# Kernel optimization log

Measured on AMD Instinct MI355X. Metric: run time of the kernel, lower is better.

Reference implementation:

```python
import jax, jax.numpy as jnp
import numpy as np

D_MODEL, D_STATE, D_CONV, EXPAND = 1024, 16, 4, 2
D_INNER = EXPAND * D_MODEL
B, L = 2, 2048
DT = 0.1  # module hard-codes dt = 0.1 (dt_proj is unused)


def setup_inputs() -> dict:
    key = jax.random.key(0)
    ks = jax.random.split(key, 7)
    s = 0.02
    x = jax.random.normal(ks[0], (B, L, D_MODEL), dtype=jnp.float32)
    in_proj_w = jax.random.normal(ks[1], (2 * D_INNER, D_MODEL), dtype=jnp.float32) * s
    conv_w = jax.random.normal(ks[2], (D_INNER, 1, D_CONV), dtype=jnp.float32) * s
    conv_b = jnp.zeros((D_INNER,), dtype=jnp.float32)
    x_proj_w = jax.random.normal(ks[3], (2 * D_STATE, D_INNER), dtype=jnp.float32) * s
    A_log = jnp.log(jnp.tile(jnp.arange(1, D_STATE + 1, dtype=jnp.float32), (D_INNER, 1)))
    D_param = jnp.ones((D_INNER,), dtype=jnp.float32)
    out_proj_w = jax.random.normal(ks[4], (D_MODEL, D_INNER), dtype=jnp.float32) * s
    return {"x": x, "in_proj_w": in_proj_w, "conv_w": conv_w, "conv_b": conv_b,
            "x_proj_w": x_proj_w, "A_log": A_log, "D_param": D_param,
            "out_proj_w": out_proj_w}


def _silu(v):
    return v * jax.nn.sigmoid(v)


def reference(x, in_proj_w, conv_w, conv_b, x_proj_w, A_log, D_param, out_proj_w):
    # in_proj: (B,L,d_model) -> (B,L,2*d_inner)
    xz = jnp.einsum('bld,ed->ble', x, in_proj_w)
    xs, z = jnp.split(xz, 2, axis=-1)
    # depthwise causal conv1d (torch pads both sides d_conv-1 then slices [:L] == left-pad only)
    xc = jax.lax.conv_general_dilated(
        xs.transpose(0, 2, 1), conv_w, window_strides=(1,),
        padding=[(D_CONV - 1, 0)], dimension_numbers=('NCH', 'OIH', 'NCH'),
        feature_group_count=D_INNER) + conv_b[None, :, None]
    xs = _silu(xc.transpose(0, 2, 1))  # (B, L, d_inner)
    # x_proj -> B_proj, C_proj  (B,L,d_state) each
    x_dbl = jnp.einsum('bld,ed->ble', xs, x_proj_w)
    B_proj, C_proj = jnp.split(x_dbl, 2, axis=-1)
    # SSM scan; dt is constant 0.1 so dA = exp(dt*A) is time-invariant
    A = -jnp.exp(A_log)                 # (d_inner, d_state)
    dA = jnp.exp(DT * A)                # (d_inner, d_state)

    def step(h, inp):
        x_t, B_t, C_t = inp             # (B,D), (B,N), (B,N)
        h = dA[None] * h + DT * B_t[:, None, :] * x_t[:, :, None]
        y_t = jnp.einsum('bdn,bn->bd', h, C_t)
        return h, y_t

    h0 = jnp.zeros((B, D_INNER, D_STATE), dtype=xs.dtype)
    _, ys = jax.lax.scan(step, h0,
                         (xs.transpose(1, 0, 2), B_proj.transpose(1, 0, 2), C_proj.transpose(1, 0, 2)))
    y = ys.transpose(1, 0, 2) + xs * D_param[None, None, :]
    y = y * _silu(z)
    return jnp.einsum('bld,ed->ble', y, out_proj_w)
```

## Files before the change

### kernel.cpp

```cpp
#include <hip/hip_runtime.h>
#include <hip/hip_bf16.h>
#include <math.h>

#define D_MODEL 1024
#define D_STATE 16
#define D_CONV  4
#define D_INNER 2048
#define BATCH   2
#define SEQ     2048
#define M_TOTAL (BATCH*SEQ)
#define DT_VAL  0.1f

#define CHUNK 64
#define WARM  64
#define NCHUNK (SEQ / CHUNK)
#define TSTEP 8

typedef __attribute__((ext_vector_type(8))) __bf16 bf16x8;
typedef __attribute__((ext_vector_type(4))) __bf16 bf16x4;
typedef __attribute__((ext_vector_type(4))) float floatx4;

__device__ __forceinline__ void gld_lds16(const __bf16* g, __bf16* l) {
    __builtin_amdgcn_global_load_lds(
        (const __attribute__((address_space(1))) void*)g,
        (__attribute__((address_space(3))) void*)l, 16, 0, 0);
}

template<int EPI>
__global__ __launch_bounds__(256) void gemm_v4(
    const __bf16* __restrict__ A, int lda,
    const __bf16* __restrict__ W, int ldw,
    float* __restrict__ Cf, int ldc,
    __bf16* __restrict__ O1, __bf16* __restrict__ O2,
    int nbx, int klen)
{
    __shared__ __bf16 As[2][128][32];
    __shared__ __bf16 Bs[2][128][32];

    const int tid  = threadIdx.x;
    const int bid  = blockIdx.x;
    const int xcd  = bid & 7;
    const int i    = bid >> 3;
    const int byl  = i & 3;
    const int rest = i >> 2;
    const int bx   = rest % nbx;
    const int ks   = rest / nbx;
    const int m0   = (xcd * 4 + byl) * 128;
    const int n0   = bx * 128;
    const int koff = ks * klen;

    const int wave = tid >> 6;
    const int lane = tid & 63;
    const int wr   = (wave >> 1) << 6;
    const int wc   = (wave & 1) << 6;
    const int fm   = lane & 15;
    const int fk   = (lane >> 4) << 3;
    const int grow = lane >> 2;
    const int gcol = (lane & 3) << 3;

    floatx4 acc[4][4];
    #pragma unroll
    for (int a = 0; a < 4; ++a)
        #pragma unroll
        for (int b = 0; b < 4; ++b)
            acc[a][b] = (floatx4){0.f, 0.f, 0.f, 0.f};

    for (int k0 = 0; k0 < klen; k0 += 64) {
        const int kg = koff + k0;
        __syncthreads();
        #pragma unroll
        for (int p = 0; p < 2; ++p) {
            #pragma unroll
            for (int issue = 0; issue < 2; ++issue) {
                const int r = issue * 64 + wave * 16 + grow;
                gld_lds16(A + (size_t)(m0 + r) * lda + kg + p * 32 + gcol,
                          &As[p][r][gcol]);
                gld_lds16(W + (size_t)(n0 + r) * ldw + kg + p * 32 + gcol,
                          &Bs[p][r][gcol]);
            }
        }
        __syncthreads();

        #pragma unroll
        for (int p = 0; p < 2; ++p) {
            bf16x8 af[4], bfv[4];
            #pragma unroll
            for (int a = 0; a < 4; ++a)
                af[a] = *(bf16x8*)&As[p][wr + a * 16 + fm][fk];
            #pragma unroll
            for (int b = 0; b < 4; ++b)
                bfv[b] = *(bf16x8*)&Bs[p][wc + b * 16 + fm][fk];
            #pragma unroll
            for (int a = 0; a < 4; ++a)
                #pragma unroll
                for (int b = 0; b < 4; ++b)
                    acc[a][b] = __builtin_amdgcn_mfma_f32_16x16x32_bf16(
                        af[a], bfv[b], acc[a][b], 0, 0, 0);
        }
    }

    const int crow = (lane >> 4) << 2;
    const int ccol = lane & 15;
    #pragma unroll
    for (int a = 0; a < 4; ++a) {
        #pragma unroll
        for (int b = 0; b < 4; ++b) {
            const int cm = m0 + wr + a * 16 + crow;
            const int cn = n0 + wc + b * 16 + ccol;
            #pragma unroll
            for (int r = 0; r < 4; ++r) {
                const float v = acc[a][b][r];
                if (EPI == 1) {
                    if (n0 < 2048) {
                        O1[(size_t)(cm + r) * 2048 + cn] = (__bf16)v;
                    } else {
                        const float s = v / (1.f + __expf(-v));
                        O2[(size_t)(cm + r) * 2048 + cn - 2048] = (__bf16)s;
                    }
                } else {
                    Cf[(size_t)ks * M_TOTAL * ldc + (size_t)(cm + r) * ldc + cn] = v;
                }
            }
        }
    }
}

__global__ __launch_bounds__(256) void reduce2(
    const float* __restrict__ p, float* __restrict__ out)
{
    const size_t i = (size_t)(blockIdx.x * 256 + threadIdx.x) * 4;
    const float4 a = *(const float4*)(p + i);
    const float4 b = *(const float4*)(p + (size_t)M_TOTAL * D_MODEL + i);
    float4 o;
    o.x = a.x + b.x; o.y = a.y + b.y; o.z = a.z + b.z; o.w = a.w + b.w;
    *(float4*)(out + i) = o;
}

__global__ __launch_bounds__(256) void xproj_mfma(
    const __bf16* __restrict__ X, const __bf16* __restrict__ Wp,
    float* __restrict__ bc)
{
    __shared__ __bf16 Ash[128][32];
    __shared__ __bf16 Wsh[32][264];

    const int tid  = threadIdx.x;
    const int bid  = blockIdx.x;
    const int ks   = bid & 7;
    const int mb   = bid >> 3;
    const int m0   = mb * 128;
    const int koff = ks * 256;
    const int wave = tid >> 6;
    const int lane = tid & 63;
    const int fm   = lane & 15;
    const int fk   = (lane >> 4) << 3;
    const int grow = lane >> 2;
    const int gcol = (lane & 3) << 3;

    {
        const int r = tid >> 3;
        const int c = (tid & 7) << 5;
        #pragma unroll
        for (int q = 0; q < 4; ++q)
            *(bf16x8*)&Wsh[r][c + q * 8] =
                *(const bf16x8*)(Wp + (size_t)r * D_INNER + koff + c + q * 8);
    }

    floatx4 acc[2][2];
    #pragma unroll
    for (int a = 0; a < 2; ++a)
        #pragma unroll
        for (int b = 0; b < 2; ++b)
            acc[a][b] = (floatx4){0.f, 0.f, 0.f, 0.f};

    for (int kit = 0; kit < 8; ++kit) {
        const int kg = koff + kit * 32;
        __syncthreads();
        #pragma unroll
        for (int issue = 0; issue < 2; ++issue) {
            const int r = issue * 64 + wave * 16 + grow;
            gld_lds16(X + (size_t)(m0 + r) * D_INNER + kg + gcol, &Ash[r][gcol]);
        }
        __syncthreads();

        bf16x8 af[2], wf[2];
        af[0] = *(bf16x8*)&Ash[wave * 32 + fm][fk];
        af[1] = *(bf16x8*)&Ash[wave * 32 + 16 + fm][fk];
        wf[0] = *(bf16x8*)&Wsh[fm][kit * 32 + fk];
        wf[1] = *(bf16x8*)&Wsh[16 + fm][kit * 32 + fk];
        #pragma unroll
        for (int a = 0; a < 2; ++a)
            #pragma unroll
            for (int b = 0; b < 2; ++b)
                acc[a][b] = __builtin_amdgcn_mfma_f32_16x16x32_bf16(
                    af[a], wf[b], acc[a][b], 0, 0, 0);
    }

    const int crow = (lane >> 4) << 2;
    const int ccol = lane & 15;
    #pragma unroll
    for (int a = 0; a < 2; ++a)
        #pragma unroll
        for (int b = 0; b < 2; ++b)
            #pragma unroll
            for (int r = 0; r < 4; ++r)
                atomicAdd(bc + (size_t)(m0 + wave * 32 + a * 16 + crow + r) * 32
                             + b * 16 + ccol, acc[a][b][r]);
}

__global__ __launch_bounds__(256) void cast4(
    const float* __restrict__ x, const float* __restrict__ win,
    const float* __restrict__ wout, const float* __restrict__ xpw,
    __bf16* __restrict__ xbf, __bf16* __restrict__ winbf,
    __bf16* __restrict__ woutbf, __bf16* __restrict__ xpwbf)
{
    const size_t j = (size_t)(blockIdx.x * 256 + threadIdx.x) * 4;
    const float* src; __bf16* dst; size_t off;
    if (j < 4194304)       { src = x;    dst = xbf;    off = j; }
    else if (j < 8388608)  { src = win;  dst = winbf;  off = j - 4194304; }
    else if (j < 10485760) { src = wout; dst = woutbf; off = j - 8388608; }
    else                   { src = xpw;  dst = xpwbf;  off = j - 10485760; }
    const float4 v = *(const float4*)(src + off);
    bf16x4 o;
    o[0] = (__bf16)v.x; o[1] = (__bf16)v.y; o[2] = (__bf16)v.z; o[3] = (__bf16)v.w;
    *(bf16x4*)(dst + off) = o;
}

__global__ __launch_bounds__(256) void conv_silu(
    const __bf16* __restrict__ xsp, const float* __restrict__ cw,
    const float* __restrict__ cb, __bf16* __restrict__ xsc)
{
    const int g  = blockIdx.x * 256 + threadIdx.x;
    const int d4 = g & (D_INNER / 4 - 1);
    const int m  = g >> 9;
    const int l  = m & (SEQ - 1);
    const int d  = d4 << 2;

    const float4 w0 = *(const float4*)(cw + (size_t)(d + 0) * 4);
    const float4 w1 = *(const float4*)(cw + (size_t)(d + 1) * 4);
    const float4 w2 = *(const float4*)(cw + (size_t)(d + 2) * 4);
    const float4 w3 = *(const float4*)(cw + (size_t)(d + 3) * 4);
    const float4 bv = *(const float4*)(cb + d);
    float a0 = bv.x, a1 = bv.y, a2 = bv.z, a3 = bv.w;

    #pragma unroll
    for (int j = 0; j < 4; ++j) {
        if (l + j >= 3) {
            const bf16x4 v = *(const bf16x4*)(xsp + (size_t)(m + j - 3) * D_INNER + d);
            const float wj0 = (j==0)?w0.x:(j==1)?w0.y:(j==2)?w0.z:w0.w;
            const float wj1 = (j==0)?w1.x:(j==1)?w1.y:(j==2)?w1.z:w1.w;
            const float wj2 = (j==0)?w2.x:(j==1)?w2.y:(j==2)?w2.z:w2.w;
            const float wj3 = (j==0)?w3.x:(j==1)?w3.y:(j==2)?w3.z:w3.w;
            a0 = fmaf(wj0, (float)v[0], a0);
            a1 = fmaf(wj1, (float)v[1], a1);
            a2 = fmaf(wj2, (float)v[2], a2);
            a3 = fmaf(wj3, (float)v[3], a3);
        }
    }
    a0 = a0 / (1.f + __expf(-a0));
    a1 = a1 / (1.f + __expf(-a1));
    a2 = a2 / (1.f + __expf(-a2));
    a3 = a3 / (1.f + __expf(-a3));
    bf16x4 ob;
    ob[0] = (__bf16)a0; ob[1] = (__bf16)a1; ob[2] = (__bf16)a2; ob[3] = (__bf16)a3;
    *(bf16x4*)(xsc + (size_t)m * D_INNER + d) = ob;
}

__global__ __launch_bounds__(256) void ssm_scan(
    const __bf16* __restrict__ xsc, const float* __restrict__ bc,
    const __bf16* __restrict__ szbf, __bf16* __restrict__ ybf,
    const float* __restrict__ alog, const float* __restrict__ dpar)
{
    __shared__ float Bsh[CHUNK + WARM][16];
    __shared__ float Csh[CHUNK + WARM][16];
    __shared__ float Xsh[2][TSTEP][256];
    __shared__ float Zsh[2][TSTEP][256];

    const int tid = threadIdx.x;
    const int blk = blockIdx.x;
    const int db  = blk & 7;
    const int ch  = (blk >> 3) & (NCHUNK - 1);
    const int b   = blk >> 8;
    const int d0  = db * 256;
    const int d   = d0 + tid;
    const int t0  = ch * CHUNK;
    const int tw  = (t0 >= WARM) ? (t0 - WARM) : 0;
    const int warm = t0 - tw;
    const int nt  = t0 + CHUNK - tw;
    const int ntiles = nt / TSTEP;

    const float* bcp = bc + ((size_t)b * SEQ + tw) * 32;
    for (int i = tid; i < nt * 8; i += 256) {
        const int row = i >> 3, q = i & 7;
        const float4 v = *(const float4*)(bcp + (size_t)row * 32 + q * 4);
        if (q < 4) *(float4*)&Bsh[row][q * 4] = v;
        else       *(float4*)&Csh[row][(q - 4) * 4] = v;
    }

    float dAv[16], h[16];
    #pragma unroll
    for (int q = 0; q < 4; ++q) {
        const float4 av = *(const float4*)(alog + (size_t)d * D_STATE + q * 4);
        dAv[q*4+0] = expf(-DT_VAL * expf(av.x));
        dAv[q*4+1] = expf(-DT_VAL * expf(av.y));
        dAv[q*4+2] = expf(-DT_VAL * expf(av.z));
        dAv[q*4+3] = expf(-DT_VAL * expf(av.w));
    }
    #pragma unroll
    for (int n = 0; n < 16; ++n) h[n] = 0.f;
    const float Dd = dpar[d];

    const __bf16* xbase = xsc  + ((size_t)b * SEQ + tw) * D_INNER + d0;
    const __bf16* zbase = szbf + ((size_t)b * SEQ + tw) * D_INNER + d0;
    __bf16*       ybase = ybf  + ((size_t)b * SEQ + tw) * D_INNER + d0;

    const int lrow = tid >> 6;
    const int lcol = (tid & 63) << 2;

    {
        const bf16x4 xa = *(const bf16x4*)(xbase + (size_t)lrow * D_INNER + lcol);
        const bf16x4 xb = *(const bf16x4*)(xbase + (size_t)(lrow + 4) * D_INNER + lcol);
        float4 fa, fb;
        fa.x=(float)xa[0]; fa.y=(float)xa[1]; fa.z=(float)xa[2]; fa.w=(float)xa[3];
        fb.x=(float)xb[0]; fb.y=(float)xb[1]; fb.z=(float)xb[2]; fb.w=(float)xb[3];
        *(float4*)&Xsh[0][lrow][lcol]     = fa;
        *(float4*)&Xsh[0][lrow + 4][lcol] = fb;
        if (warm == 0) {
            const bf16x4 za = *(const bf16x4*)(zbase + (size_t)lrow * D_INNER + lcol);
            const bf16x4 zb = *(const bf16x4*)(zbase + (size_t)(lrow + 4) * D_INNER + lcol);
            float4 ga, gb;
            ga.x=(float)za[0]; ga.y=(float)za[1]; ga.z=(float)za[2]; ga.w=(float)za[3];
            gb.x=(float)zb[0]; gb.y=(float)zb[1]; gb.z=(float)zb[2]; gb.w=(float)zb[3];
            *(float4*)&Zsh[0][lrow][lcol]     = ga;
            *(float4*)&Zsh[0][lrow + 4][lcol] = gb;
        }
    }
    __syncthreads();

    for (int tile = 0; tile < ntiles; ++tile) {
        const int buf = tile & 1;
        const int s   = tile * TSTEP;
        const int s2  = s + TSTEP;
        const bool more = (tile + 1 < ntiles);
        const bool znext = more && (s2 >= warm);

        bf16x4 rx0, rx1, rz0, rz1;
        if (more) {
            rx0 = *(const bf16x4*)(xbase + (size_t)(s2 + lrow) * D_INNER + lcol);
            rx1 = *(const bf16x4*)(xbase + (size_t)(s2 + lrow + 4) * D_INNER + lcol);
        }
        if (znext) {
            rz0 = *(const bf16x4*)(zbase + (size_t)(s2 + lrow) * D_INNER + lcol);
            rz1 = *(const bf16x4*)(zbase + (size_t)(s2 + lrow + 4) * D_INNER + lcol);
        }

        #pragma unroll
        for (int tt = 0; tt < TSTEP; ++tt) {
            const int t = s + tt;
            const float x   = Xsh[buf][tt][tid];
            const float dtx = DT_VAL * x;
            float y0 = 0.f, y1 = 0.f, y2 = 0.f, y3 = 0.f;
            #pragma unroll
            for (int n = 0; n < 4; ++n) {
                h[n]      = fmaf(dAv[n],      h[n],      dtx * Bsh[t][n]);
                h[n + 4]  = fmaf(dAv[n + 4],  h[n + 4],  dtx * Bsh[t][n + 4]);
                h[n + 8]  = fmaf(dAv[n + 8],  h[n + 8],  dtx * Bsh[t][n + 8]);
                h[n + 12] = fmaf(dAv[n + 12], h[n + 12], dtx * Bsh[t][n + 12]);
                y0 = fmaf(h[n],      Csh[t][n],      y0);
                y1 = fmaf(h[n + 4],  Csh[t][n + 4],  y1);
                y2 = fmaf(h[n + 8],  Csh[t][n + 8],  y2);
                y3 = fmaf(h[n + 12], Csh[t][n + 12], y3);
            }
            if (t >= warm) {
                const float sz = Zsh[buf][tt][tid];
                const float y  = fmaf(x, Dd, (y0 + y1) + (y2 + y3));
                ybase[(size_t)t * D_INNER + tid] = (__bf16)(y * sz);
            }
        }

        if (more) {
            float4 fa, fb;
            fa.x=(float)rx0[0]; fa.y=(float)rx0[1]; fa.z=(float)rx0[2]; fa.w=(float)rx0[3];
            fb.x=(float)rx1[0]; fb.y=(float)rx1[1]; fb.z=(float)rx1[2]; fb.w=(float)rx1[3];
            *(float4*)&Xsh[buf ^ 1][lrow][lcol]     = fa;
            *(float4*)&Xsh[buf ^ 1][lrow + 4][lcol] = fb;
        }
        if (znext) {
            float4 ga, gb;
            ga.x=(float)rz0[0]; ga.y=(float)rz0[1]; ga.z=(float)rz0[2]; ga.w=(float)rz0[3];
            gb.x=(float)rz1[0]; gb.y=(float)rz1[1]; gb.z=(float)rz1[2]; gb.w=(float)rz1[3];
            *(float4*)&Zsh[buf ^ 1][lrow][lcol]     = ga;
            *(float4*)&Zsh[buf ^ 1][lrow + 4][lcol] = gb;
        }
        __syncthreads();
    }
}

extern "C" void kernel_launch(void* const* d_in, const int* in_sizes, int n_in,
                              void* d_out, int out_size, void* d_ws, size_t ws_size,
                              hipStream_t stream)
{
    const float* x    = (const float*)d_in[0];
    const float* win  = (const float*)d_in[1];
    const float* cw   = (const float*)d_in[2];
    const float* cb   = (const float*)d_in[3];
    const float* xpw  = (const float*)d_in[4];
    const float* alog = (const float*)d_in[5];
    const float* dpar = (const float*)d_in[6];
    const float* wout = (const float*)d_in[7];
    float* out = (float*)d_out;

    char* w = (char*)d_ws;
    float*  pbuf   = (float*)w;
    __bf16* szbf   = (__bf16*)(w + 33554432);
    __bf16* xspbf  = (__bf16*)(w + 50331648);
    __bf16* xsc    = (__bf16*)(w + 67108864);
    float*  bcbuf  = (float*)(w + 83886080);
    __bf16* r1     = (__bf16*)(w + 84410368);
    __bf16* xbf    = r1;
    __bf16* winbf  = r1 + 4194304;
    __bf16* ybf    = r1;
    __bf16* woutbf = (__bf16*)(w + 101187584);
    __bf16* xpwbf  = (__bf16*)(w + 105381888);

    cast4<<<10304, 256, 0, stream>>>(x, win, wout, xpw, xbf, winbf, woutbf, xpwbf);
    hipMemsetAsync(bcbuf, 0, (size_t)M_TOTAL * 32 * 4, stream);
    gemm_v4<1><<<1024, 256, 0, stream>>>(
        xbf, D_MODEL, winbf, D_MODEL, nullptr, 0, xspbf, szbf, 32, 1024);
    conv_silu<<<(M_TOTAL * (D_INNER / 4)) / 256, 256, 0, stream>>>(
        xspbf, cw, cb, xsc);
    xproj_mfma<<<256, 256, 0, stream>>>(xsc, xpwbf, bcbuf);
    ssm_scan<<<BATCH * NCHUNK * 8, 256, 0, stream>>>(
        xsc, bcbuf, szbf, ybf, alog, dpar);
    gemm_v4<2><<<512, 256, 0, stream>>>(
        ybf, D_INNER, woutbf, D_INNER, pbuf, D_MODEL, nullptr, nullptr, 8, 1024);
    reduce2<<<(M_TOTAL * D_MODEL / 4) / 256, 256, 0, stream>>>(pbuf, out);
}
```

Baseline: 258.9 us.

## Use 256x128 tile GEMM for in_proj and fold bc memset into cast kernel

Adds a dedicated in_proj GEMM kernel with 256x128 output tiles per block (each wave computes 128x64), halving the block count to 512 and raising arithmetic intensity per LDS load. The zeroing of the B/C accumulation buffer moves from a separate hipMemsetAsync into extra threads of the cast kernel, removing one launch. The larger per-wave accumulator (32 MFMA tiles) raises register pressure and may reduce occupancy.

```diff
diff --git a/kernel.cpp b/kernel.cpp
--- a/kernel.cpp
+++ b/kernel.cpp
@@ -26,12 +26,101 @@
         (__attribute__((address_space(3))) void*)l, 16, 0, 0);
 }
 
-template<int EPI>
+__global__ __launch_bounds__(256) void gemm_inproj_fat(
+    const __bf16* __restrict__ A, const __bf16* __restrict__ W,
+    __bf16* __restrict__ O1, __bf16* __restrict__ O2)
+{
+    __shared__ __bf16 As[2][256][32];
+    __shared__ __bf16 Bs[2][128][32];
+
+    const int tid  = threadIdx.x;
+    const int bid  = blockIdx.x;
+    const int xcd  = bid & 7;
+    const int i    = bid >> 3;
+    const int byl  = i & 1;
+    const int bx   = i >> 1;
+    const int m0   = (xcd * 2 + byl) * 256;
+    const int n0   = bx * 128;
+
+    const int wave = tid >> 6;
+    const int lane = tid & 63;
+    const int wm   = (wave >> 1) << 7;
+    const int wn   = (wave & 1) << 6;
+    const int fm   = lane & 15;
+    const int fk   = (lane >> 4) << 3;
+    const int grow = lane >> 2;
+    const int gcol = (lane & 3) << 3;
+
+    floatx4 acc[8][4];
+    #pragma unroll
+    for (int a = 0; a < 8; ++a)
+        #pragma unroll
+        for (int b = 0; b < 4; ++b)
+            acc[a][b] = (floatx4){0.f, 0.f, 0.f, 0.f};
+
+    for (int kg = 0; kg < D_MODEL; kg += 64) {
+        __syncthreads();
+        #pragma unroll
+        for (int p = 0; p < 2; ++p) {
+            #pragma unroll
+            for (int issue = 0; issue < 4; ++issue) {
+                const int r = issue * 64 + wave * 16 + grow;
+                gld_lds16(A + (size_t)(m0 + r) * D_MODEL + kg + p * 32 + gcol,
+                          &As[p][r][gcol]);
+            }
+            #pragma unroll
+            for (int issue = 0; issue < 2; ++issue) {
+                const int r = issue * 64 + wave * 16 + grow;
+                gld_lds16(W + (size_t)(n0 + r) * D_MODEL + kg + p * 32 + gcol,
+                          &Bs[p][r][gcol]);
+            }
+        }
+        __syncthreads();
+
+        #pragma unroll
+        for (int p = 0; p < 2; ++p) {
+            bf16x8 af[8], bfv[4];
+            #pragma unroll
+            for (int a = 0; a < 8; ++a)
+                af[a] = *(bf16x8*)&As[p][wm + a * 16 + fm][fk];
+            #pragma unroll
+            for (int b = 0; b < 4; ++b)
+                bfv[b] = *(bf16x8*)&Bs[p][wn + b * 16 + fm][fk];
+            #pragma unroll
+            for (int a = 0; a < 8; ++a)
+                #pragma unroll
+                for (int b = 0; b < 4; ++b)
+                    acc[a][b] = __builtin_amdgcn_mfma_f32_16x16x32_bf16(
+                        af[a], bfv[b], acc[a][b], 0, 0, 0);
+        }
+    }
+
+    const int crow = (lane >> 4) << 2;
+    const int ccol = lane & 15;
+    #pragma unroll
+    for (int a = 0; a < 8; ++a) {
+        #pragma unroll
+        for (int b = 0; b < 4; ++b) {
+            const int cm = m0 + wm + a * 16 + crow;
+            const int cn = n0 + wn + b * 16 + ccol;
+            #pragma unroll
+            for (int r = 0; r < 4; ++r) {
+                const float v = acc[a][b][r];
+                if (n0 < 2048) {
+                    O1[(size_t)(cm + r) * 2048 + cn] = (__bf16)v;
+                } else {
+                    const float s = v / (1.f + __expf(-v));
+                    O2[(size_t)(cm + r) * 2048 + cn - 2048] = (__bf16)s;
+                }
+            }
+        }
+    }
+}
+
 __global__ __launch_bounds__(256) void gemm_v4(
     const __bf16* __restrict__ A, int lda,
     const __bf16* __restrict__ W, int ldw,
     float* __restrict__ Cf, int ldc,
-    __bf16* __restrict__ O1, __bf16* __restrict__ O2,
     int nbx, int klen)
 {
     __shared__ __bf16 As[2][128][32];
@@ -108,19 +197,9 @@
             const int cm = m0 + wr + a * 16 + crow;
             const int cn = n0 + wc + b * 16 + ccol;
             #pragma unroll
-            for (int r = 0; r < 4; ++r) {
-                const float v = acc[a][b][r];
-                if (EPI == 1) {
-                    if (n0 < 2048) {
-                        O1[(size_t)(cm + r) * 2048 + cn] = (__bf16)v;
-                    } else {
-                        const float s = v / (1.f + __expf(-v));
-                        O2[(size_t)(cm + r) * 2048 + cn - 2048] = (__bf16)s;
-                    }
-                } else {
-                    Cf[(size_t)ks * M_TOTAL * ldc + (size_t)(cm + r) * ldc + cn] = v;
-                }
-            }
+            for (int r = 0; r < 4; ++r)
+                Cf[(size_t)ks * M_TOTAL * ldc + (size_t)(cm + r) * ldc + cn] =
+                    acc[a][b][r];
         }
     }
 }
@@ -207,13 +286,20 @@
                              + b * 16 + ccol, acc[a][b][r]);
 }
 
-__global__ __launch_bounds__(256) void cast4(
+__global__ __launch_bounds__(256) void cast5(
     const float* __restrict__ x, const float* __restrict__ win,
     const float* __restrict__ wout, const float* __restrict__ xpw,
     __bf16* __restrict__ xbf, __bf16* __restrict__ winbf,
-    __bf16* __restrict__ woutbf, __bf16* __restrict__ xpwbf)
-{
-    const size_t j = (size_t)(blockIdx.x * 256 + threadIdx.x) * 4;
+    __bf16* __restrict__ woutbf, __bf16* __restrict__ xpwbf,
+    float* __restrict__ bcz)
+{
+    const size_t g = (size_t)(blockIdx.x * 256 + threadIdx.x);
+    if (g >= 2637824) {
+        const size_t off = (g - 2637824) * 4;
+        *(float4*)(bcz + off) = (float4){0.f, 0.f, 0.f, 0.f};
+        return;
+    }
+    const size_t j = g * 4;
     const float* src; __bf16* dst; size_t off;
     if (j < 4194304)       { src = x;    dst = xbf;    off = j; }
     else if (j < 8388608)  { src = win;  dst = winbf;  off = j - 4194304; }
@@ -422,16 +508,15 @@
     __bf16* woutbf = (__bf16*)(w + 101187584);
     __bf16* xpwbf  = (__bf16*)(w + 105381888);
 
-    cast4<<<10304, 256, 0, stream>>>(x, win, wout, xpw, xbf, winbf, woutbf, xpwbf);
-    hipMemsetAsync(bcbuf, 0, (size_t)M_TOTAL * 32 * 4, stream);
-    gemm_v4<1><<<1024, 256, 0, stream>>>(
-        xbf, D_MODEL, winbf, D_MODEL, nullptr, 0, xspbf, szbf, 32, 1024);
+    cast5<<<10432, 256, 0, stream>>>(x, win, wout, xpw,
+                                     xbf, winbf, woutbf, xpwbf, bcbuf);
+    gemm_inproj_fat<<<512, 256, 0, stream>>>(xbf, winbf, xspbf, szbf);
     conv_silu<<<(M_TOTAL * (D_INNER / 4)) / 256, 256, 0, stream>>>(
         xspbf, cw, cb, xsc);
     xproj_mfma<<<256, 256, 0, stream>>>(xsc, xpwbf, bcbuf);
     ssm_scan<<<BATCH * NCHUNK * 8, 256, 0, stream>>>(
         xsc, bcbuf, szbf, ybf, alog, dpar);
-    gemm_v4<2><<<512, 256, 0, stream>>>(
-        ybf, D_INNER, woutbf, D_INNER, pbuf, D_MODEL, nullptr, nullptr, 8, 1024);
+    gemm_v4<<<512, 256, 0, stream>>>(
+        ybf, D_INNER, woutbf, D_INNER, pbuf, D_MODEL, 8, 1024);
     reduce2<<<(M_TOTAL * D_MODEL / 4) / 256, 256, 0, stream>>>(pbuf, out);
 }
```

Result: slower. 286.8 us (+10.8%).

## Template GEMM dims, use 4-way split-K for out_proj, fold memset into cast

Applied to the files above, without the earlier changes.

Turns the GEMM's leading dimensions, K length and tile-column count into template constants and hoists the load address arithmetic out of the k-loop. The out_proj GEMM now splits K four ways instead of two, doubling its grid to 1024 blocks, with partials stored in two buffers (one reusing dead workspace) and summed by a four-input reduction. The hipMemset of the B/C accumulator is folded into the cast kernel to save a launch. The larger split gives better CU occupancy on the out_proj GEMM but writes and reads twice as much partial-sum traffic.

```diff
diff --git a/kernel.cpp b/kernel.cpp
--- a/kernel.cpp
+++ b/kernel.cpp
@@ -26,13 +26,11 @@
         (__attribute__((address_space(3))) void*)l, 16, 0, 0);
 }
 
-template<int EPI>
-__global__ __launch_bounds__(256) void gemm_v4(
-    const __bf16* __restrict__ A, int lda,
-    const __bf16* __restrict__ W, int ldw,
-    float* __restrict__ Cf, int ldc,
-    __bf16* __restrict__ O1, __bf16* __restrict__ O2,
-    int nbx, int klen)
+template<int EPI, int LDA, int LDW, int KLEN, int NBX>
+__global__ __launch_bounds__(256) void gemm_v5(
+    const __bf16* __restrict__ A, const __bf16* __restrict__ W,
+    float* __restrict__ Cf, float* __restrict__ Cf2, int ldc,
+    __bf16* __restrict__ O1, __bf16* __restrict__ O2)
 {
     __shared__ __bf16 As[2][128][32];
     __shared__ __bf16 Bs[2][128][32];
@@ -43,11 +41,11 @@
     const int i    = bid >> 3;
     const int byl  = i & 3;
     const int rest = i >> 2;
-    const int bx   = rest % nbx;
-    const int ks   = rest / nbx;
+    const int bx   = rest % NBX;
+    const int ks   = rest / NBX;
     const int m0   = (xcd * 4 + byl) * 128;
     const int n0   = bx * 128;
-    const int koff = ks * klen;
+    const int koff = ks * KLEN;
 
     const int wave = tid >> 6;
     const int lane = tid & 63;
@@ -65,19 +63,18 @@
         for (int b = 0; b < 4; ++b)
             acc[a][b] = (floatx4){0.f, 0.f, 0.f, 0.f};
 
-    for (int k0 = 0; k0 < klen; k0 += 64) {
-        const int kg = koff + k0;
+    const __bf16* ap = A + (size_t)(m0 + wave * 16 + grow) * LDA + koff + gcol;
+    const __bf16* wp = W + (size_t)(n0 + wave * 16 + grow) * LDW + koff + gcol;
+    const int arow = wave * 16 + grow;
+
+    for (int k0 = 0; k0 < KLEN; k0 += 64) {
         __syncthreads();
         #pragma unroll
         for (int p = 0; p < 2; ++p) {
-            #pragma unroll
-            for (int issue = 0; issue < 2; ++issue) {
-                const int r = issue * 64 + wave * 16 + grow;
-                gld_lds16(A + (size_t)(m0 + r) * lda + kg + p * 32 + gcol,
-                          &As[p][r][gcol]);
-                gld_lds16(W + (size_t)(n0 + r) * ldw + kg + p * 32 + gcol,
-                          &Bs[p][r][gcol]);
-            }
+            gld_lds16(ap + k0 + p * 32,                    &As[p][arow][gcol]);
+            gld_lds16(ap + k0 + p * 32 + (size_t)64 * LDA, &As[p][arow + 64][gcol]);
+            gld_lds16(wp + k0 + p * 32,                    &Bs[p][arow][gcol]);
+            gld_lds16(wp + k0 + p * 32 + (size_t)64 * LDW, &Bs[p][arow + 64][gcol]);
         }
         __syncthreads();
 
@@ -118,21 +115,29 @@
                         O2[(size_t)(cm + r) * 2048 + cn - 2048] = (__bf16)s;
                     }
                 } else {
-                    Cf[(size_t)ks * M_TOTAL * ldc + (size_t)(cm + r) * ldc + cn] = v;
+                    float* dst = (ks < 2 ? Cf : Cf2) +
+                                 (size_t)(ks & 1) * M_TOTAL * ldc;
+                    dst[(size_t)(cm + r) * ldc + cn] = v;
                 }
             }
         }
     }
 }
 
-__global__ __launch_bounds__(256) void reduce2(
-    const float* __restrict__ p, float* __restrict__ out)
+__global__ __launch_bounds__(256) void reduce4(
+    const float* __restrict__ p01, const float* __restrict__ p23,
+    float* __restrict__ out)
 {
     const size_t i = (size_t)(blockIdx.x * 256 + threadIdx.x) * 4;
-    const float4 a = *(const float4*)(p + i);
-    const float4 b = *(const float4*)(p + (size_t)M_TOTAL * D_MODEL + i);
+    const float4 a = *(const float4*)(p01 + i);
+    const float4 b = *(const float4*)(p01 + (size_t)M_TOTAL * D_MODEL + i);
+    const float4 c = *(const float4*)(p23 + i);
+    const float4 d = *(const float4*)(p23 + (size_t)M_TOTAL * D_MODEL + i);
     float4 o;
-    o.x = a.x + b.x; o.y = a.y + b.y; o.z = a.z + b.z; o.w = a.w + b.w;
+    o.x = (a.x + b.x) + (c.x + d.x);
+    o.y = (a.y + b.y) + (c.y + d.y);
+    o.z = (a.z + b.z) + (c.z + d.z);
+    o.w = (a.w + b.w) + (c.w + d.w);
     *(float4*)(out + i) = o;
 }
 
@@ -207,13 +212,20 @@
                              + b * 16 + ccol, acc[a][b][r]);
 }
 
-__global__ __launch_bounds__(256) void cast4(
+__global__ __launch_bounds__(256) void cast5(
     const float* __restrict__ x, const float* __restrict__ win,
     const float* __restrict__ wout, const float* __restrict__ xpw,
     __bf16* __restrict__ xbf, __bf16* __restrict__ winbf,
-    __bf16* __restrict__ woutbf, __bf16* __restrict__ xpwbf)
-{
-    const size_t j = (size_t)(blockIdx.x * 256 + threadIdx.x) * 4;
+    __bf16* __restrict__ woutbf, __bf16* __restrict__ xpwbf,
+    float* __restrict__ bcz)
+{
+    const size_t g = (size_t)(blockIdx.x * 256 + threadIdx.x);
+    if (g >= 2637824) {
+        const size_t off = (g - 2637824) * 4;
+        *(float4*)(bcz + off) = (float4){0.f, 0.f, 0.f, 0.f};
+        return;
+    }
+    const size_t j = g * 4;
     const float* src; __bf16* dst; size_t off;
     if (j < 4194304)       { src = x;    dst = xbf;    off = j; }
     else if (j < 8388608)  { src = win;  dst = winbf;  off = j - 4194304; }
@@ -414,6 +426,7 @@
     __bf16* szbf   = (__bf16*)(w + 33554432);
     __bf16* xspbf  = (__bf16*)(w + 50331648);
     __bf16* xsc    = (__bf16*)(w + 67108864);
+    float*  pbuf2  = (float*)(w + 50331648);
     float*  bcbuf  = (float*)(w + 83886080);
     __bf16* r1     = (__bf16*)(w + 84410368);
     __bf16* xbf    = r1;
@@ -422,16 +435,16 @@
     __bf16* woutbf = (__bf16*)(w + 101187584);
     __bf16* xpwbf  = (__bf16*)(w + 105381888);
 
-    cast4<<<10304, 256, 0, stream>>>(x, win, wout, xpw, xbf, winbf, woutbf, xpwbf);
-    hipMemsetAsync(bcbuf, 0, (size_t)M_TOTAL * 32 * 4, stream);
-    gemm_v4<1><<<1024, 256, 0, stream>>>(
-        xbf, D_MODEL, winbf, D_MODEL, nullptr, 0, xspbf, szbf, 32, 1024);
+    cast5<<<10432, 256, 0, stream>>>(x, win, wout, xpw,
+                                     xbf, winbf, woutbf, xpwbf, bcbuf);
+    gemm_v5<1, 1024, 1024, 1024, 32><<<1024, 256, 0, stream>>>(
+        xbf, winbf, nullptr, nullptr, 0, xspbf, szbf);
     conv_silu<<<(M_TOTAL * (D_INNER / 4)) / 256, 256, 0, stream>>>(
         xspbf, cw, cb, xsc);
     xproj_mfma<<<256, 256, 0, stream>>>(xsc, xpwbf, bcbuf);
     ssm_scan<<<BATCH * NCHUNK * 8, 256, 0, stream>>>(
         xsc, bcbuf, szbf, ybf, alog, dpar);
-    gemm_v4<2><<<512, 256, 0, stream>>>(
-        ybf, D_INNER, woutbf, D_INNER, pbuf, D_MODEL, nullptr, nullptr, 8, 1024);
-    reduce2<<<(M_TOTAL * D_MODEL / 4) / 256, 256, 0, stream>>>(pbuf, out);
-}
+    gemm_v5<2, 2048, 2048, 512, 8><<<1024, 256, 0, stream>>>(
+        ybf, woutbf, pbuf, pbuf2, D_MODEL, nullptr, nullptr);
+    reduce4<<<(M_TOTAL * D_MODEL / 4) / 256, 256, 0, stream>>>(pbuf, pbuf2, out);
+}
```

After: 259.5 us. No clear change (+0.2%).
